# Kernel optimization log

Hardware: AMD Instinct MI355X
Metric: run time of the kernel (lower is better)

Reference implementation:

```python
import jax, jax.numpy as jnp
import numpy as np

K = 7          # local attention kernel size
PAD = 3        # (K-1)//2 so output spatial dims match input
GROUPS = 8

def unfold2d(x, k):
    # x: [B, C, H+k-1, W+k-1] -> patches [B, C, H, W, k*k] (kh-major, kw-minor, matching F.unfold)
    B, C, Hp, Wp = x.shape
    H, W = Hp - k + 1, Wp - k + 1
    return jnp.stack([x[:, :, i:i + H, j:j + W] for i in range(k) for j in range(k)], axis=-1)

def setup_inputs():
    key = jax.random.key(0)
    k1, k2, k3, k4, k5, k6 = jax.random.split(key, 6)
    B, Cin, H, W = 2, 256, 56, 56
    outc = 256
    scale = (2.0 / Cin) ** 0.5  # kaiming fan_out-ish init
    return {
        "feature_map": jax.random.normal(k1, (B, 2 * Cin, H, W), jnp.float32),
        "w_q": jax.random.normal(k2, (outc, Cin), jnp.float32) * scale,
        "w_k": jax.random.normal(k3, (outc, Cin), jnp.float32) * scale,
        "w_v": jax.random.normal(k4, (outc, Cin), jnp.float32) * scale,
        "rel_h": jax.random.normal(k5, (outc // 2, K), jnp.float32),
        "rel_w": jax.random.normal(k6, (outc // 2, K), jnp.float32),
    }

def reference(feature_map, w_q, w_k, w_v, rel_h, rel_w):
    B, C2, H, W = feature_map.shape
    Cin = C2 // 2
    fm_t0, fm_t1 = feature_map[:, :Cin], feature_map[:, Cin:]
    outc = w_q.shape[0]
    # 1x1 convs (bias=False)
    q = jnp.einsum('oc,bchw->bohw', w_q, fm_t1)                      # [B, outc, H, W]
    padded = jnp.pad(fm_t0, ((0, 0), (0, 0), (PAD, PAD), (PAD, PAD)))
    kk = jnp.einsum('oc,bchw->bohw', w_k, padded)
    vv = jnp.einsum('oc,bchw->bohw', w_v, padded)
    k_out = unfold2d(kk, K)                                          # [B, outc, H, W, K*K]
    v_out = unfold2d(vv, K)
    # relative position bias: first half channels get row bias, second half col bias
    half = outc // 2
    bias_h = jnp.broadcast_to(rel_h[:, :, None], (half, K, K)).reshape(half, K * K)
    bias_w = jnp.broadcast_to(rel_w[:, None, :], (half, K, K)).reshape(half, K * K)
    bias = jnp.concatenate([bias_h, bias_w], axis=0)                 # [outc, K*K]
    k_out = k_out + bias[None, :, None, None, :]
    G, Cg = GROUPS, outc // GROUPS
    qg = q.reshape(B, G, Cg, H, W)
    kg = k_out.reshape(B, G, Cg, H, W, K * K)
    vg = v_out.reshape(B, G, Cg, H, W, K * K)
    logits = jnp.einsum('bgchw,bgchwk->bghwk', qg, kg)
    wts = jax.nn.softmax(logits, axis=-1)
    out = jnp.einsum('bghwk,bgchwk->bgchw', wts, vg)
    return out.reshape(B, outc, H, W)
```

## Files before the change

### kernel.cpp

```cpp
#include <hip/hip_runtime.h>
#include <hip/hip_bf16.h>

#define B    2
#define CIN  256
#define H    56
#define W    56
#define OUTC 256
#define KS   7
#define PAD  3
#define G    8
#define CG   32
#define HP   62
#define WP   62
#define P1   (H * W)
#define P2   (HP * WP)

typedef __attribute__((ext_vector_type(2))) _Float16 h2;
typedef __attribute__((ext_vector_type(8))) _Float16 f16x8;
typedef __attribute__((ext_vector_type(4))) float f32x4;

__device__ inline unsigned short f2h(float f) {
    const _Float16 h = (_Float16)f;
    return *(const unsigned short*)&h;
}

__device__ inline float fdot2(h2 a, h2 b, float c) {
#if defined(__has_builtin)
#if __has_builtin(__builtin_amdgcn_fdot2)
    return __builtin_amdgcn_fdot2(a, b, c, false);
#else
    return c + (float)a[0] * (float)b[0] + (float)a[1] * (float)b[1];
#endif
#else
    return c + (float)a[0] * (float)b[0] + (float)a[1] * (float)b[1];
#endif
}

__device__ inline float dot8(const f16x8 q, const f16x8 k, float s) {
    s = fdot2((h2){q[0], q[1]}, (h2){k[0], k[1]}, s);
    s = fdot2((h2){q[2], q[3]}, (h2){k[2], k[3]}, s);
    s = fdot2((h2){q[4], q[5]}, (h2){k[4], k[5]}, s);
    s = fdot2((h2){q[6], q[7]}, (h2){k[6], k[7]}, s);
    return s;
}

#define ASTR 40
__global__ __launch_bounds__(256, 2) void gemm_kernel(const float* __restrict__ fm,
                                                      const float* __restrict__ wq,
                                                      const float* __restrict__ wk,
                                                      const float* __restrict__ wv,
                                                      unsigned short* __restrict__ qi,
                                                      unsigned short* __restrict__ ki,
                                                      unsigned short* __restrict__ vi) {
    const int b = blockIdx.z;
    const bool isQ = blockIdx.y < 2;
    if (isQ && blockIdx.x >= 25) return;
    const int o0 = (isQ ? blockIdx.y : (blockIdx.y - 2)) * 128;
    const int n0 = blockIdx.x * 128;
    const int Nreal = isQ ? P1 : P2;
    const int Pstr  = isQ ? P1 : P2;

    const float* Wsrc;
    int orow0;
    if (isQ)            { Wsrc = wq; orow0 = o0; }
    else if (o0 < 256)  { Wsrc = wk; orow0 = o0; }
    else                { Wsrc = wv; orow0 = o0 - 256; }

    __shared__ unsigned short Alds[2][128 * ASTR];
    __shared__ unsigned short Blds[2][128 * ASTR];
    const int tid = threadIdx.x;
    const int lane = tid & 63;
    const int wave = tid >> 6;
    const int wr = (wave >> 1) * 64;
    const int wc = (wave & 1) * 64;
    const int lrow = lane & 15;
    const int quad = lane >> 4;

    const int arow = tid & 127;
    const int akc  = (tid >> 7) * 16;

    const int n = n0 + arow;
    int srcoff = -1;
    if (isQ) {
        if (n < P1) srcoff = n;
    } else {
        if (n < P2) {
            const int y = n / WP, x = n - y * WP;
            const int iy = y - PAD, ix = x - PAD;
            if (iy >= 0 && iy < H && ix >= 0 && ix < W) srcoff = iy * W + ix;
        }
    }
    const float* fmB = fm + ((size_t)b * (2 * CIN) + (isQ ? CIN : 0)) * P1;
    const float* wrow = Wsrc + (size_t)orow0 * CIN + (size_t)arow * CIN + akc;

    f32x4 acc[4][4] = {};

    float av[16], bv[16];
    {
        const float4 a0 = ((const float4*)wrow)[0];
        const float4 a1 = ((const float4*)wrow)[1];
        const float4 a2 = ((const float4*)wrow)[2];
        const float4 a3 = ((const float4*)wrow)[3];
        av[0]=a0.x; av[1]=a0.y; av[2]=a0.z; av[3]=a0.w;
        av[4]=a1.x; av[5]=a1.y; av[6]=a1.z; av[7]=a1.w;
        av[8]=a2.x; av[9]=a2.y; av[10]=a2.z; av[11]=a2.w;
        av[12]=a3.x; av[13]=a3.y; av[14]=a3.z; av[15]=a3.w;
        #pragma unroll
        for (int j = 0; j < 16; ++j)
            bv[j] = (srcoff >= 0) ? fmB[(size_t)(akc + j) * P1 + srcoff] : 0.f;
    }

    for (int kb = 0; kb < CIN / 32; ++kb) {
        const int cur = kb & 1;
        unsigned short* alp = Alds[cur] + arow * ASTR + akc;
        unsigned short* blp = Blds[cur] + arow * ASTR + akc;
        {
            f16x8 p0, p1, p2, p3;
            #pragma unroll
            for (int j = 0; j < 8; ++j) {
                p0[j] = (_Float16)av[j];
                p1[j] = (_Float16)av[8 + j];
                p2[j] = (_Float16)bv[j];
                p3[j] = (_Float16)bv[8 + j];
            }
            *(f16x8*)(alp)     = p0;
            *(f16x8*)(alp + 8) = p1;
            *(f16x8*)(blp)     = p2;
            *(f16x8*)(blp + 8) = p3;
        }
        __syncthreads();
        if (kb < CIN / 32 - 1) {
            const int c0 = (kb + 1) * 32 + akc;
            const float* wnext = wrow + (kb + 1) * 32;
            const float4 a0 = ((const float4*)wnext)[0];
            const float4 a1 = ((const float4*)wnext)[1];
            const float4 a2 = ((const float4*)wnext)[2];
            const float4 a3 = ((const float4*)wnext)[3];
            av[0]=a0.x; av[1]=a0.y; av[2]=a0.z; av[3]=a0.w;
            av[4]=a1.x; av[5]=a1.y; av[6]=a1.z; av[7]=a1.w;
            av[8]=a2.x; av[9]=a2.y; av[10]=a2.z; av[11]=a2.w;
            av[12]=a3.x; av[13]=a3.y; av[14]=a3.z; av[15]=a3.w;
            #pragma unroll
            for (int j = 0; j < 16; ++j)
                bv[j] = (srcoff >= 0) ? fmB[(size_t)(c0 + j) * P1 + srcoff] : 0.f;
        }
        f16x8 af[4], bfr[4];
        #pragma unroll
        for (int mi = 0; mi < 4; ++mi)
            af[mi] = *(const f16x8*)&Alds[cur][(wr + mi * 16 + lrow) * ASTR + quad * 8];
        #pragma unroll
        for (int ni = 0; ni < 4; ++ni)
            bfr[ni] = *(const f16x8*)&Blds[cur][(wc + ni * 16 + lrow) * ASTR + quad * 8];
        #pragma unroll
        for (int mi = 0; mi < 4; ++mi)
            #pragma unroll
            for (int ni = 0; ni < 4; ++ni)
                acc[mi][ni] = __builtin_amdgcn_mfma_f32_16x16x32_f16(af[mi], bfr[ni], acc[mi][ni], 0, 0, 0);
    }

    #pragma unroll
    for (int mi = 0; mi < 4; ++mi) {
        const int gmBase = o0 + wr + mi * 16 + quad * 4;
        int ch0;
        unsigned short* base;
        if (isQ)               { ch0 = gmBase;       base = qi; }
        else if (gmBase < 256) { ch0 = gmBase;       base = ki; }
        else                   { ch0 = gmBase - 256; base = vi; }
        const int g   = ch0 >> 5;
        const int sub = (ch0 >> 3) & 3;
        const int l8  = ch0 & 7;
        unsigned short* pbase = base + ((((size_t)b * 8 + g) * 4 + sub) * Pstr) * 8 + l8;
        #pragma unroll
        for (int ni = 0; ni < 4; ++ni) {
            const int gn = n0 + wc + ni * 16 + lrow;
            if (gn < Nreal) {
                ushort4 pk;
                pk.x = f2h(acc[mi][ni][0]);
                pk.y = f2h(acc[mi][ni][1]);
                pk.z = f2h(acc[mi][ni][2]);
                pk.w = f2h(acc[mi][ni][3]);
                *(ushort4*)(pbase + (size_t)gn * 8) = pk;
            }
        }
    }
}

#define NPOS4 496
#define HALFE 992
__global__ __launch_bounds__(128) void attn_kernel(const unsigned short* __restrict__ qi,
                                                   const unsigned short* __restrict__ ki,
                                                   const unsigned short* __restrict__ vi,
                                                   const float* __restrict__ rel_h,
                                                   const float* __restrict__ rel_w,
                                                   float* __restrict__ out) {
    __shared__ f16x8 sbuf[2 * HALFE];

    const int b  = blockIdx.z;
    const int g  = blockIdx.y;
    const int r0 = blockIdx.x * 2;
    const int oc0 = g * CG;
    const int tid = threadIdx.x;
    const bool active = tid < 56;
    const int cx = tid;
    const int pix0 = r0 * W + cx;
    const int pix1 = pix0 + W;

    const size_t bg4 = ((size_t)b * 8 + g) * 4;
    const size_t rowoff8 = ((size_t)r0 * WP) * 8;

    f16x8* bufA = sbuf;
    f16x8* bufB = sbuf + HALFE;

    f16x8 qh0[4], qh1[4];
    if (active) {
        #pragma unroll
        for (int sub = 0; sub < 4; ++sub) {
            qh0[sub] = *(const f16x8*)(qi + ((bg4 + sub) * P1 + pix0) * 8);
            qh1[sub] = *(const f16x8*)(qi + ((bg4 + sub) * P1 + pix1) * 8);
        }
    }

    f16x8 st[8];
    {
        const unsigned short* gb = ki + bg4 * P2 * 8 + rowoff8;
        #pragma unroll
        for (int it = 0; it < 8; ++it) {
            const int e = tid + it * 128;
            if (e < HALFE) {
                const int sl = (e >= NPOS4);
                const int pos = e - (sl ? NPOS4 : 0);
                st[it] = *(const f16x8*)(gb + ((size_t)sl * P2 + pos) * 8);
            }
        }
        #pragma unroll
        for (int it = 0; it < 8; ++it) {
            const int e = tid + it * 128;
            if (e < HALFE) bufA[e] = st[it];
        }
    }
    __syncthreads();

    {
        const unsigned short* gb = ki + (bg4 + 2) * P2 * 8 + rowoff8;
        #pragma unroll
        for (int it = 0; it < 8; ++it) {
            const int e = tid + it * 128;
            if (e < HALFE) {
                const int sl = (e >= NPOS4);
                const int pos = e - (sl ? NPOS4 : 0);
                st[it] = *(const f16x8*)(gb + ((size_t)sl * P2 + pos) * 8);
            }
        }
    }

    float logits0[KS * KS], logits1[KS * KS];
    if (active) {
        const float* rel = (g < 4) ? (rel_h + oc0 * KS) : (rel_w + (oc0 - 128) * KS);
        float qf0[32], qf1[32];
        #pragma unroll
        for (int sub = 0; sub < 4; ++sub)
            #pragma unroll
            for (int j = 0; j < 8; ++j) {
                qf0[sub * 8 + j] = (float)qh0[sub][j];
                qf1[sub * 8 + j] = (float)qh1[sub][j];
            }
        float bd0[KS], bd1[KS];
        #pragma unroll
        for (int t = 0; t < KS; ++t) {
            float s0 = 0.f, s1 = 0.f;
            #pragma unroll
            for (int c = 0; c < 32; ++c) {
                const float r = rel[c * KS + t];
                s0 += qf0[c] * r;
                s1 += qf1[c] * r;
            }
            bd0[t] = s0; bd1[t] = s1;
        }
        #pragma unroll
        for (int i = 0; i < KS; ++i)
            #pragma unroll
            for (int j = 0; j < KS; ++j) {
                logits0[i * KS + j] = (g < 4) ? bd0[i] : bd0[j];
                logits1[i * KS + j] = (g < 4) ? bd1[i] : bd1[j];
            }

        #pragma unroll
        for (int s = 0; s < 2; ++s) {
            const f16x8 q0 = qh0[s];
            const f16x8 q1 = qh1[s];
            #pragma unroll
            for (int j = 0; j < KS; ++j) {
                #pragma unroll
                for (int ii = 0; ii < 8; ++ii) {
                    const f16x8 kv = bufA[s * NPOS4 + ii * WP + cx + j];
                    if (ii < 7)  logits0[ii * KS + j]       = dot8(q0, kv, logits0[ii * KS + j]);
                    if (ii >= 1) logits1[(ii - 1) * KS + j] = dot8(q1, kv, logits1[(ii - 1) * KS + j]);
                }
            }
        }
    }
    #pragma unroll
    for (int it = 0; it < 8; ++it) {
        const int e = tid + it * 128;
        if (e < HALFE) bufB[e] = st[it];
    }
    __syncthreads();

    {
        const unsigned short* gb = vi + bg4 * P2 * 8 + rowoff8;
        #pragma unroll
        for (int it = 0; it < 8; ++it) {
            const int e = tid + it * 128;
            if (e < HALFE) {
                const int sl = (e >= NPOS4);
                const int pos = e - (sl ? NPOS4 : 0);
                st[it] = *(const f16x8*)(gb + ((size_t)sl * P2 + pos) * 8);
            }
        }
    }

    if (active) {
        #pragma unroll
        for (int s = 0; s < 2; ++s) {
            const f16x8 q0 = qh0[2 + s];
            const f16x8 q1 = qh1[2 + s];
            #pragma unroll
            for (int j = 0; j < KS; ++j) {
                #pragma unroll
                for (int ii = 0; ii < 8; ++ii) {
                    const f16x8 kv = bufB[s * NPOS4 + ii * WP + cx + j];
                    if (ii < 7)  logits0[ii * KS + j]       = dot8(q0, kv, logits0[ii * KS + j]);
                    if (ii >= 1) logits1[(ii - 1) * KS + j] = dot8(q1, kv, logits1[(ii - 1) * KS + j]);
                }
            }
        }
        {
            float m = logits0[0];
            #pragma unroll
            for (int t = 1; t < KS * KS; ++t) m = fmaxf(m, logits0[t]);
            float sum = 0.f;
            #pragma unroll
            for (int t = 0; t < KS * KS; ++t) {
                const float e = __expf(logits0[t] - m);
                logits0[t] = e;
                sum += e;
            }
            const float inv = 1.f / sum;
            #pragma unroll
            for (int t = 0; t < KS * KS; ++t) logits0[t] *= inv;
        }
        {
            float m = logits1[0];
            #pragma unroll
            for (int t = 1; t < KS * KS; ++t) m = fmaxf(m, logits1[t]);
            float sum = 0.f;
            #pragma unroll
            for (int t = 0; t < KS * KS; ++t) {
                const float e = __expf(logits1[t] - m);
                logits1[t] = e;
                sum += e;
            }
            const float inv = 1.f / sum;
            #pragma unroll
            for (int t = 0; t < KS * KS; ++t) logits1[t] *= inv;
        }
    }
    #pragma unroll
    for (int it = 0; it < 8; ++it) {
        const int e = tid + it * 128;
        if (e < HALFE) bufA[e] = st[it];
    }
    __syncthreads();

    {
        const unsigned short* gb = vi + (bg4 + 2) * P2 * 8 + rowoff8;
        #pragma unroll
        for (int it = 0; it < 8; ++it) {
            const int e = tid + it * 128;
            if (e < HALFE) {
                const int sl = (e >= NPOS4);
                const int pos = e - (sl ? NPOS4 : 0);
                st[it] = *(const f16x8*)(gb + ((size_t)sl * P2 + pos) * 8);
            }
        }
    }

    if (active) {
        #pragma unroll
        for (int s = 0; s < 2; ++s) {
            float a0[8] = {}, a1[8] = {};
            #pragma unroll
            for (int j = 0; j < KS; ++j) {
                #pragma unroll
                for (int ii = 0; ii < 8; ++ii) {
                    const f16x8 v = bufA[s * NPOS4 + ii * WP + cx + j];
                    if (ii < 7) {
                        const float wt = logits0[ii * KS + j];
                        #pragma unroll
                        for (int c = 0; c < 8; ++c) a0[c] += wt * (float)v[c];
                    }
                    if (ii >= 1) {
                        const float wt = logits1[(ii - 1) * KS + j];
                        #pragma unroll
                        for (int c = 0; c < 8; ++c) a1[c] += wt * (float)v[c];
                    }
                }
            }
            float* op0 = out + ((size_t)b * OUTC + oc0 + s * 8) * P1 + pix0;
            float* op1 = out + ((size_t)b * OUTC + oc0 + s * 8) * P1 + pix1;
            #pragma unroll
            for (int c = 0; c < 8; ++c) {
                op0[(size_t)c * P1] = a0[c];
                op1[(size_t)c * P1] = a1[c];
            }
        }
    }
    #pragma unroll
    for (int it = 0; it < 8; ++it) {
        const int e = tid + it * 128;
        if (e < HALFE) bufB[e] = st[it];
    }
    __syncthreads();

    if (active) {
        #pragma unroll
        for (int s = 0; s < 2; ++s) {
            float a0[8] = {}, a1[8] = {};
            #pragma unroll
            for (int j = 0; j < KS; ++j) {
                #pragma unroll
                for (int ii = 0; ii < 8; ++ii) {
                    const f16x8 v = bufB[s * NPOS4 + ii * WP + cx + j];
                    if (ii < 7) {
                        const float wt = logits0[ii * KS + j];
                        #pragma unroll
                        for (int c = 0; c < 8; ++c) a0[c] += wt * (float)v[c];
                    }
                    if (ii >= 1) {
                        const float wt = logits1[(ii - 1) * KS + j];
                        #pragma unroll
                        for (int c = 0; c < 8; ++c) a1[c] += wt * (float)v[c];
                    }
                }
            }
            float* op0 = out + ((size_t)b * OUTC + oc0 + 16 + s * 8) * P1 + pix0;
            float* op1 = out + ((size_t)b * OUTC + oc0 + 16 + s * 8) * P1 + pix1;
            #pragma unroll
            for (int c = 0; c < 8; ++c) {
                op0[(size_t)c * P1] = a0[c];
                op1[(size_t)c * P1] = a1[c];
            }
        }
    }
}

extern "C" void kernel_launch(void* const* d_in, const int* in_sizes, int n_in,
                              void* d_out, int out_size, void* d_ws, size_t ws_size,
                              hipStream_t stream) {
    const float* fm = (const float*)d_in[0];
    const float* wq = (const float*)d_in[1];
    const float* wk = (const float*)d_in[2];
    const float* wv = (const float*)d_in[3];
    const float* rh = (const float*)d_in[4];
    const float* rw = (const float*)d_in[5];
    float* out = (float*)d_out;

    unsigned short* ws = (unsigned short*)d_ws;
    unsigned short* qi = ws;
    unsigned short* ki = qi + (size_t)B * OUTC * P1;
    unsigned short* vi = ki + (size_t)B * OUTC * P2;

    gemm_kernel<<<dim3(31, 6, B), 256, 0, stream>>>(fm, wq, wk, wv, qi, ki, vi);
    attn_kernel<<<dim3(H / 2, G, B), 128, 0, stream>>>(qi, ki, vi, rh, rw, out);
}
```

Measured before the change: 108.6 us.

## Load all K and V tiles into shared memory up front with one barrier

Replaces the four-stage register-staged double-buffer pipeline in the attention kernel with a single bulk load of all K and V channel slices into shared memory, followed by one barrier. Inactive threads now exit early. The goal is to cut the number of barriers and serialized phases and to issue all global loads at once for more memory-level parallelism. In exchange, shared memory per block rises from about 32 KB to 64 KB and many more registers are held for staging, which can lower occupancy. The overlap between loading and compute is also lost.

```diff
diff --git a/kernel.cpp b/kernel.cpp
--- a/kernel.cpp
+++ b/kernel.cpp
@@ -185,15 +185,14 @@
     }
 }
 
-#define NPOS4 496
-#define HALFE 992
+#define NPOS 496
 __global__ __launch_bounds__(128) void attn_kernel(const unsigned short* __restrict__ qi,
                                                    const unsigned short* __restrict__ ki,
                                                    const unsigned short* __restrict__ vi,
                                                    const float* __restrict__ rel_h,
                                                    const float* __restrict__ rel_w,
                                                    float* __restrict__ out) {
-    __shared__ f16x8 sbuf[2 * HALFE];
+    __shared__ f16x8 sbuf[8 * NPOS];
 
     const int b  = blockIdx.z;
     const int g  = blockIdx.y;
@@ -206,10 +205,10 @@
     const int pix1 = pix0 + W;
 
     const size_t bg4 = ((size_t)b * 8 + g) * 4;
-    const size_t rowoff8 = ((size_t)r0 * WP) * 8;
-
-    f16x8* bufA = sbuf;
-    f16x8* bufB = sbuf + HALFE;
+    const int woff = r0 * WP;
+
+    f16x8* bufK = sbuf;
+    f16x8* bufV = sbuf + 4 * NPOS;
 
     f16x8 qh0[4], qh1[4];
     if (active) {
@@ -220,41 +219,45 @@
         }
     }
 
-    f16x8 st[8];
+    f16x8 stK[16], stV[16];
+    #pragma unroll
+    for (int sub = 0; sub < 4; ++sub) {
+        const unsigned short* gk = ki + ((bg4 + sub) * P2 + woff) * 8;
+        #pragma unroll
+        for (int it = 0; it < 4; ++it) {
+            const int e = tid + it * 128;
+            if (e < NPOS) stK[sub * 4 + it] = *(const f16x8*)(gk + (size_t)e * 8);
+        }
+    }
+    #pragma unroll
+    for (int sub = 0; sub < 4; ++sub) {
+        const unsigned short* gv = vi + ((bg4 + sub) * P2 + woff) * 8;
+        #pragma unroll
+        for (int it = 0; it < 4; ++it) {
+            const int e = tid + it * 128;
+            if (e < NPOS) stV[sub * 4 + it] = *(const f16x8*)(gv + (size_t)e * 8);
+        }
+    }
+    #pragma unroll
+    for (int sub = 0; sub < 4; ++sub)
+        #pragma unroll
+        for (int it = 0; it < 4; ++it) {
+            const int e = tid + it * 128;
+            if (e < NPOS) bufK[sub * NPOS + e] = stK[sub * 4 + it];
+        }
+    #pragma unroll
+    for (int sub = 0; sub < 4; ++sub)
+        #pragma unroll
+        for (int it = 0; it < 4; ++it) {
+            const int e = tid + it * 128;
+            if (e < NPOS) bufV[sub * NPOS + e] = stV[sub * 4 + it];
+        }
+    __syncthreads();
+
+    if (!active) return;
+
+    float logits0[KS * KS], logits1[KS * KS];
     {
-        const unsigned short* gb = ki + bg4 * P2 * 8 + rowoff8;
-        #pragma unroll
-        for (int it = 0; it < 8; ++it) {
-            const int e = tid + it * 128;
-            if (e < HALFE) {
-                const int sl = (e >= NPOS4);
-                const int pos = e - (sl ? NPOS4 : 0);
-                st[it] = *(const f16x8*)(gb + ((size_t)sl * P2 + pos) * 8);
-            }
-        }
-        #pragma unroll
-        for (int it = 0; it < 8; ++it) {
-            const int e = tid + it * 128;
-            if (e < HALFE) bufA[e] = st[it];
-        }
-    }
-    __syncthreads();
-
-    {
-        const unsigned short* gb = ki + (bg4 + 2) * P2 * 8 + rowoff8;
-        #pragma unroll
-        for (int it = 0; it < 8; ++it) {
-            const int e = tid + it * 128;
-            if (e < HALFE) {
-                const int sl = (e >= NPOS4);
-                const int pos = e - (sl ? NPOS4 : 0);
-                st[it] = *(const f16x8*)(gb + ((size_t)sl * P2 + pos) * 8);
-            }
-        }
-    }
-
-    float logits0[KS * KS], logits1[KS * KS];
-    if (active) {
         const float* rel = (g < 4) ? (rel_h + oc0 * KS) : (rel_w + (oc0 - 128) * KS);
         float qf0[32], qf1[32];
         #pragma unroll
@@ -283,173 +286,80 @@
                 logits0[i * KS + j] = (g < 4) ? bd0[i] : bd0[j];
                 logits1[i * KS + j] = (g < 4) ? bd1[i] : bd1[j];
             }
-
-        #pragma unroll
-        for (int s = 0; s < 2; ++s) {
-            const f16x8 q0 = qh0[s];
-            const f16x8 q1 = qh1[s];
-            #pragma unroll
-            for (int j = 0; j < KS; ++j) {
-                #pragma unroll
-                for (int ii = 0; ii < 8; ++ii) {
-                    const f16x8 kv = bufA[s * NPOS4 + ii * WP + cx + j];
-                    if (ii < 7)  logits0[ii * KS + j]       = dot8(q0, kv, logits0[ii * KS + j]);
-                    if (ii >= 1) logits1[(ii - 1) * KS + j] = dot8(q1, kv, logits1[(ii - 1) * KS + j]);
+    }
+
+    #pragma unroll
+    for (int s = 0; s < 4; ++s) {
+        const f16x8 q0 = qh0[s];
+        const f16x8 q1 = qh1[s];
+        #pragma unroll
+        for (int j = 0; j < KS; ++j) {
+            #pragma unroll
+            for (int ii = 0; ii < 8; ++ii) {
+                const f16x8 kv = bufK[s * NPOS + ii * WP + cx + j];
+                if (ii < 7)  logits0[ii * KS + j]       = dot8(q0, kv, logits0[ii * KS + j]);
+                if (ii >= 1) logits1[(ii - 1) * KS + j] = dot8(q1, kv, logits1[(ii - 1) * KS + j]);
+            }
+        }
+    }
+
+    {
+        float m = logits0[0];
+        #pragma unroll
+        for (int t = 1; t < KS * KS; ++t) m = fmaxf(m, logits0[t]);
+        float sum = 0.f;
+        #pragma unroll
+        for (int t = 0; t < KS * KS; ++t) {
+            const float e = __expf(logits0[t] - m);
+            logits0[t] = e;
+            sum += e;
+        }
+        const float inv = 1.f / sum;
+        #pragma unroll
+        for (int t = 0; t < KS * KS; ++t) logits0[t] *= inv;
+    }
+    {
+        float m = logits1[0];
+        #pragma unroll
+        for (int t = 1; t < KS * KS; ++t) m = fmaxf(m, logits1[t]);
+        float sum = 0.f;
+        #pragma unroll
+        for (int t = 0; t < KS * KS; ++t) {
+            const float e = __expf(logits1[t] - m);
+            logits1[t] = e;
+            sum += e;
+        }
+        const float inv = 1.f / sum;
+        #pragma unroll
+        for (int t = 0; t < KS * KS; ++t) logits1[t] *= inv;
+    }
+
+    #pragma unroll
+    for (int s = 0; s < 4; ++s) {
+        float a0[8] = {}, a1[8] = {};
+        #pragma unroll
+        for (int j = 0; j < KS; ++j) {
+            #pragma unroll
+            for (int ii = 0; ii < 8; ++ii) {
+                const f16x8 v = bufV[s * NPOS + ii * WP + cx + j];
+                if (ii < 7) {
+                    const float wt = logits0[ii * KS + j];
+                    #pragma unroll
+                    for (int c = 0; c < 8; ++c) a0[c] += wt * (float)v[c];
                 }
-            }
-        }
-    }
-    #pragma unroll
-    for (int it = 0; it < 8; ++it) {
-        const int e = tid + it * 128;
-        if (e < HALFE) bufB[e] = st[it];
-    }
-    __syncthreads();
-
-    {
-        const unsigned short* gb = vi + bg4 * P2 * 8 + rowoff8;
-        #pragma unroll
-        for (int it = 0; it < 8; ++it) {
-            const int e = tid + it * 128;
-            if (e < HALFE) {
-                const int sl = (e >= NPOS4);
-                const int pos = e - (sl ? NPOS4 : 0);
-                st[it] = *(const f16x8*)(gb + ((size_t)sl * P2 + pos) * 8);
-            }
-        }
-    }
-
-    if (active) {
-        #pragma unroll
-        for (int s = 0; s < 2; ++s) {
-            const f16x8 q0 = qh0[2 + s];
-            const f16x8 q1 = qh1[2 + s];
-            #pragma unroll
-            for (int j = 0; j < KS; ++j) {
-                #pragma unroll
-                for (int ii = 0; ii < 8; ++ii) {
-                    const f16x8 kv = bufB[s * NPOS4 + ii * WP + cx + j];
-                    if (ii < 7)  logits0[ii * KS + j]       = dot8(q0, kv, logits0[ii * KS + j]);
-                    if (ii >= 1) logits1[(ii - 1) * KS + j] = dot8(q1, kv, logits1[(ii - 1) * KS + j]);
+                if (ii >= 1) {
+                    const float wt = logits1[(ii - 1) * KS + j];
+                    #pragma unroll
+                    for (int c = 0; c < 8; ++c) a1[c] += wt * (float)v[c];
                 }
             }
         }
-        {
-            float m = logits0[0];
-            #pragma unroll
-            for (int t = 1; t < KS * KS; ++t) m = fmaxf(m, logits0[t]);
-            float sum = 0.f;
-            #pragma unroll
-            for (int t = 0; t < KS * KS; ++t) {
-                const float e = __expf(logits0[t] - m);
-                logits0[t] = e;
-                sum += e;
-            }
-            const float inv = 1.f / sum;
-            #pragma unroll
-            for (int t = 0; t < KS * KS; ++t) logits0[t] *= inv;
-        }
-        {
-            float m = logits1[0];
-            #pragma unroll
-            for (int t = 1; t < KS * KS; ++t) m = fmaxf(m, logits1[t]);
-            float sum = 0.f;
-            #pragma unroll
-            for (int t = 0; t < KS * KS; ++t) {
-                const float e = __expf(logits1[t] - m);
-                logits1[t] = e;
-                sum += e;
-            }
-            const float inv = 1.f / sum;
-            #pragma unroll
-            for (int t = 0; t < KS * KS; ++t) logits1[t] *= inv;
-        }
-    }
-    #pragma unroll
-    for (int it = 0; it < 8; ++it) {
-        const int e = tid + it * 128;
-        if (e < HALFE) bufA[e] = st[it];
-    }
-    __syncthreads();
-
-    {
-        const unsigned short* gb = vi + (bg4 + 2) * P2 * 8 + rowoff8;
-        #pragma unroll
-        for (int it = 0; it < 8; ++it) {
-            const int e = tid + it * 128;
-            if (e < HALFE) {
-                const int sl = (e >= NPOS4);
-                const int pos = e - (sl ? NPOS4 : 0);
-                st[it] = *(const f16x8*)(gb + ((size_t)sl * P2 + pos) * 8);
-            }
-        }
-    }
-
-    if (active) {
-        #pragma unroll
-        for (int s = 0; s < 2; ++s) {
-            float a0[8] = {}, a1[8] = {};
-            #pragma unroll
-            for (int j = 0; j < KS; ++j) {
-                #pragma unroll
-                for (int ii = 0; ii < 8; ++ii) {
-                    const f16x8 v = bufA[s * NPOS4 + ii * WP + cx + j];
-                    if (ii < 7) {
-                        const float wt = logits0[ii * KS + j];
-                        #pragma unroll
-                        for (int c = 0; c < 8; ++c) a0[c] += wt * (float)v[c];
-                    }
-                    if (ii >= 1) {
-                        const float wt = logits1[(ii - 1) * KS + j];
-                        #pragma unroll
-                        for (int c = 0; c < 8; ++c) a1[c] += wt * (float)v[c];
-                    }
-                }
-            }
-            float* op0 = out + ((size_t)b * OUTC + oc0 + s * 8) * P1 + pix0;
-            float* op1 = out + ((size_t)b * OUTC + oc0 + s * 8) * P1 + pix1;
-            #pragma unroll
-            for (int c = 0; c < 8; ++c) {
-                op0[(size_t)c * P1] = a0[c];
-                op1[(size_t)c * P1] = a1[c];
-            }
-        }
-    }
-    #pragma unroll
-    for (int it = 0; it < 8; ++it) {
-        const int e = tid + it * 128;
-        if (e < HALFE) bufB[e] = st[it];
-    }
-    __syncthreads();
-
-    if (active) {
-        #pragma unroll
-        for (int s = 0; s < 2; ++s) {
-            float a0[8] = {}, a1[8] = {};
-            #pragma unroll
-            for (int j = 0; j < KS; ++j) {
-                #pragma unroll
-                for (int ii = 0; ii < 8; ++ii) {
-                    const f16x8 v = bufB[s * NPOS4 + ii * WP + cx + j];
-                    if (ii < 7) {
-                        const float wt = logits0[ii * KS + j];
-                        #pragma unroll
-                        for (int c = 0; c < 8; ++c) a0[c] += wt * (float)v[c];
-                    }
-                    if (ii >= 1) {
-                        const float wt = logits1[(ii - 1) * KS + j];
-                        #pragma unroll
-                        for (int c = 0; c < 8; ++c) a1[c] += wt * (float)v[c];
-                    }
-                }
-            }
-            float* op0 = out + ((size_t)b * OUTC + oc0 + 16 + s * 8) * P1 + pix0;
-            float* op1 = out + ((size_t)b * OUTC + oc0 + 16 + s * 8) * P1 + pix1;
-            #pragma unroll
-            for (int c = 0; c < 8; ++c) {
-                op0[(size_t)c * P1] = a0[c];
-                op1[(size_t)c * P1] = a1[c];
-            }
+        float* op0 = out + ((size_t)b * OUTC + oc0 + s * 8) * P1 + pix0;
+        float* op1 = out + ((size_t)b * OUTC + oc0 + s * 8) * P1 + pix1;
+        #pragma unroll
+        for (int c = 0; c < 8; ++c) {
+            op0[(size_t)c * P1] = a0[c];
+            op1[(size_t)c * P1] = a1[c];
         }
     }
 }
```

New measurement: 112.4 us. +3.4%, slower.
